# Kernel optimization log

Hardware: AMD Instinct MI355X
Metric: run time of the kernel (lower is better)

## Reference

```python
import jax, jax.numpy as jnp
import numpy as np

D_IN = 768
D_OUT = 768
N_HEADS = 12
HEAD_DIM = D_OUT // N_HEADS


def setup_inputs() -> dict:
    key = jax.random.key(0)
    ks = jax.random.split(key, 6)
    B, S = 2, 4096
    x = jax.random.normal(ks[0], (B, S, D_IN), dtype=jnp.float32)
    s = 0.02
    Wq = jax.random.normal(ks[1], (D_IN, D_OUT), dtype=jnp.float32) * s
    Wk = jax.random.normal(ks[2], (D_IN, D_OUT), dtype=jnp.float32) * s
    Wv = jax.random.normal(ks[3], (D_IN, D_OUT), dtype=jnp.float32) * s
    Wo = jax.random.normal(ks[4], (D_OUT, D_OUT), dtype=jnp.float32) * s
    bo = jnp.zeros((D_OUT,), dtype=jnp.float32)
    return {"x": x, "Wq": Wq, "Wk": Wk, "Wv": Wv, "Wo": Wo, "bo": bo}


def reference(x, Wq, Wk, Wv, Wo, bo):
    B, S, _ = x.shape
    # QKV projections (no bias), reshape to [B, H, S, Dh]
    q = (x @ Wq).reshape(B, S, N_HEADS, HEAD_DIM).transpose(0, 2, 1, 3)
    k = (x @ Wk).reshape(B, S, N_HEADS, HEAD_DIM).transpose(0, 2, 1, 3)
    v = (x @ Wv).reshape(B, S, N_HEADS, HEAD_DIM).transpose(0, 2, 1, 3)
    # scores: [B, H, S, S], causal mask, scaled softmax
    scores = jnp.einsum('bhqd,bhkd->bhqk', q, k)
    causal = jnp.triu(jnp.ones((S, S), dtype=bool), k=1)
    scores = jnp.where(causal, -jnp.inf, scores)
    attn = jax.nn.softmax(scores / np.sqrt(HEAD_DIM).astype(np.float32), axis=-1)
    # dropout p=0.0 -> identity
    ctx = jnp.einsum('bhqk,bhkd->bqhd', attn, v).reshape(B, S, D_OUT)
    return ctx @ Wo + bo
```

## Files before the change

### kernel.cpp

```cpp
#include <hip/hip_runtime.h>

#define S 4096
#define BATCH 2
#define D 768
#define NH 12
#define DH 64
#define NROWS (BATCH * S)
#define N_ITEMS (32 * NH * BATCH)
#define CTR_OFF 67633152

typedef __attribute__((ext_vector_type(8))) short bf16x8;
typedef __attribute__((ext_vector_type(4))) float f32x4;
typedef __attribute__((ext_vector_type(2))) unsigned uint32x2;

__device__ __forceinline__ unsigned short f2bf(float f) {
    unsigned u = __builtin_bit_cast(unsigned, f);
    u += 0x7fff + ((u >> 16) & 1);
    return (unsigned short)(u >> 16);
}

__device__ __forceinline__ float fexp2(float x) {
#if __has_builtin(__builtin_amdgcn_exp2f)
    return __builtin_amdgcn_exp2f(x);
#else
    return exp2f(x);
#endif
}

#define GLDS16(g, l)                                                   \
    __builtin_amdgcn_global_load_lds(                                  \
        (const __attribute__((address_space(1))) void*)(g),            \
        (__attribute__((address_space(3))) void*)(l), 16, 0, 0)

__global__ __launch_bounds__(256) void cvt_x(const float* __restrict__ x,
                                             unsigned short* __restrict__ xb)
{
    int i = (blockIdx.x * 256 + threadIdx.x) * 4;
    float4 v = *(const float4*)(x + i);
    ushort4 o = make_ushort4(f2bf(v.x), f2bf(v.y), f2bf(v.z), f2bf(v.w));
    *(ushort4*)(xb + i) = o;
}

__global__ __launch_bounds__(256) void cvt_w(
    const float* __restrict__ Wq, const float* __restrict__ Wk,
    const float* __restrict__ Wv, const float* __restrict__ Wo,
    unsigned short* __restrict__ wt)
{
    __shared__ float tile[32][33];
    const int z = blockIdx.z;
    const float* W = (z == 0) ? Wq : (z == 1) ? Wk : (z == 2) ? Wv : Wo;
    const int k0 = blockIdx.x * 32, n0 = blockIdx.y * 32;
    const int t = threadIdx.x;
    const int r = t >> 3, c4 = (t & 7) * 4;

    float4 v = *(const float4*)(W + (size_t)(k0 + r) * D + n0 + c4);
    tile[r][c4 + 0] = v.x; tile[r][c4 + 1] = v.y;
    tile[r][c4 + 2] = v.z; tile[r][c4 + 3] = v.w;
    __syncthreads();
    ushort4 o = make_ushort4(f2bf(tile[c4 + 0][r]), f2bf(tile[c4 + 1][r]),
                             f2bf(tile[c4 + 2][r]), f2bf(tile[c4 + 3][r]));
    *(ushort4*)(wt + ((size_t)z * D + n0 + r) * D + k0 + c4) = o;
}

__global__ __launch_bounds__(256) void gemm_qkv(
    const unsigned short* __restrict__ xb,
    const unsigned short* __restrict__ wt,
    unsigned short* __restrict__ qb, unsigned short* __restrict__ kb,
    unsigned short* __restrict__ vtb)
{
    __shared__ unsigned short As[128 * 64];
    __shared__ unsigned short Bs[128 * 64];

    const int t = threadIdx.x;
    const int lane = t & 63, w = t >> 6;
    const int l16 = lane & 15, quad = lane >> 4;
    const int wm = w & 1, wn = w >> 1;
    const int m0 = blockIdx.x * 128;
    const int n0g = blockIdx.y * 128;
    const int z = n0g / 768;
    const int c0 = n0g - z * 768;
    const unsigned short* Wz = wt + (size_t)z * D * D;

    f32x4 acc[4][4] = {};

    for (int k0 = 0; k0 < D; k0 += 64) {
#pragma unroll
        for (int i = 0; i < 4; ++i) {
            int g = i * 256 + w * 64 + lane;
            int row = g >> 3, cl = g & 7, cg = cl ^ (row & 7);
            GLDS16(xb + (size_t)(m0 + row) * D + k0 + cg * 8,
                   As + (size_t)(i * 256 + w * 64) * 8);
            GLDS16(Wz + (size_t)(c0 + row) * D + k0 + cg * 8,
                   Bs + (size_t)(i * 256 + w * 64) * 8);
        }
        __syncthreads();
#pragma unroll
        for (int kk = 0; kk < 2; ++kk) {
            bf16x8 af[4], bf_[4];
#pragma unroll
            for (int mt = 0; mt < 4; ++mt) {
                int r = wm * 64 + mt * 16 + l16;
                int c = kk * 4 + quad;
                af[mt] = *(const bf16x8*)&As[(r * 8 + (c ^ (r & 7))) * 8];
            }
#pragma unroll
            for (int nt = 0; nt < 4; ++nt) {
                int r = wn * 64 + nt * 16 + l16;
                int c = kk * 4 + quad;
                bf_[nt] = *(const bf16x8*)&Bs[(r * 8 + (c ^ (r & 7))) * 8];
            }
#pragma unroll
            for (int mt = 0; mt < 4; ++mt)
#pragma unroll
                for (int nt = 0; nt < 4; ++nt)
                    acc[mt][nt] = __builtin_amdgcn_mfma_f32_16x16x32_bf16(
                        af[mt], bf_[nt], acc[mt][nt], 0, 0, 0);
        }
        __syncthreads();
    }

    if (z < 2) {
        unsigned short* outp = (z == 0) ? qb : kb;
        const float scale = (z == 0) ? 0.18033688011112042f : 1.0f;
#pragma unroll
        for (int mt = 0; mt < 4; ++mt) {
#pragma unroll
            for (int reg = 0; reg < 4; ++reg) {
                int m = wm * 64 + mt * 16 + quad * 4 + reg;
                int ng = m0 + m;
                int b = ng >> 12, s = ng & 4095;
#pragma unroll
                for (int nt = 0; nt < 4; ++nt) {
                    int n = c0 + wn * 64 + nt * 16 + l16;
                    int h = n >> 6, dh = n & 63;
                    outp[(((size_t)b * NH + h) * S + s) * DH + dh] =
                        f2bf(acc[mt][nt][reg] * scale);
                }
            }
        }
    } else {
#pragma unroll
        for (int mt = 0; mt < 4; ++mt) {
#pragma unroll
            for (int nt = 0; nt < 4; ++nt) {
                int m = wm * 64 + mt * 16 + quad * 4;
                int ng = m0 + m;
                int b = ng >> 12, s = ng & 4095;
                int n = c0 + wn * 64 + nt * 16 + l16;
                int h = n >> 6, dh = n & 63;
                ushort4 p = make_ushort4(
                    f2bf(acc[mt][nt][0]), f2bf(acc[mt][nt][1]),
                    f2bf(acc[mt][nt][2]), f2bf(acc[mt][nt][3]));
                *(ushort4*)(vtb + (((size_t)b * NH + h) * DH + dh) * S + s) = p;
            }
        }
    }
}

__global__ __launch_bounds__(512, 4) void attn_mfma(
    const unsigned short* __restrict__ qg,
    const unsigned short* __restrict__ kg,
    const unsigned short* __restrict__ vtg,
    unsigned short* __restrict__ ctxb,
    int* __restrict__ work_ctr)
{
    __shared__ unsigned short Ks[2][64 * 64];
    __shared__ unsigned short Vs[2][64 * 64];
    __shared__ int s_item;

    const float INF = __builtin_inff();
    const int t = threadIdx.x;
    const int w = t >> 6, lane = t & 63;
    const int l16 = lane & 15, quad = lane >> 4;
    const int a7 = l16 & 7;
    const int srow = t >> 3;
    const int scg = (t & 7) ^ (srow & 7);

    bf16x8 vone;
#pragma unroll
    for (int i = 0; i < 8; ++i) vone[i] = (short)0x3F80;

    for (;;) {
        if (t == 0) s_item = atomicAdd(work_ctr, 1);
        __syncthreads();
        const int p = s_item;
        if (p >= N_ITEMS) return;

        const int qt = 31 - (p / (NH * BATCH));
        const int hb = p % (NH * BATCH);
        const int h = hb % NH, b = hb / NH;
        const size_t hbase = ((size_t)b * NH + h) * (size_t)S * DH;
        const unsigned short* kp = kg + hbase;
        const unsigned short* vp = vtg + hbase;

        const int qrow = qt * 128 + w * 16 + l16;
        bf16x8 bq[2];
#pragma unroll
        for (int kk = 0; kk < 2; ++kk)
            bq[kk] = *(const bf16x8*)(qg + hbase + (size_t)qrow * DH +
                                      kk * 32 + quad * 8);

        f32x4 acc_o[4] = {};
        f32x4 acc_sum = {};

        const int jmax = 2 * qt + 1, jd = 2 * qt;

        GLDS16(kp + (size_t)srow * DH + scg * 8, &Ks[0][(size_t)w * 64 * 8]);
        GLDS16(vp + (size_t)srow * S + scg * 8, &Vs[0][(size_t)w * 64 * 8]);

        for (int j = 0; j <= jmax; ++j) {
            const int cur = j & 1;
            __syncthreads();
            if (j < jmax) {
                GLDS16(kp + (size_t)((j + 1) * 64 + srow) * DH + scg * 8,
                       &Ks[cur ^ 1][(size_t)w * 64 * 8]);
                GLDS16(vp + (size_t)srow * S + (j + 1) * 64 + scg * 8,
                       &Vs[cur ^ 1][(size_t)w * 64 * 8]);
            }

            const unsigned short* Kc = Ks[cur];
            const unsigned short* Vc = Vs[cur];

            f32x4 acc_s[4] = {};
            __builtin_amdgcn_s_setprio(1);
#pragma unroll
            for (int kk = 0; kk < 2; ++kk)
#pragma unroll
                for (int ms = 0; ms < 4; ++ms) {
                    int r = ms * 16 + l16, c = kk * 4 + quad;
                    bf16x8 ak = *(const bf16x8*)&Kc[(r * 8 + (c ^ a7)) * 8];
                    acc_s[ms] = __builtin_amdgcn_mfma_f32_16x16x32_bf16(
                        ak, bq[kk], acc_s[ms], 0, 0, 0);
                }
            __builtin_amdgcn_s_setprio(0);

            if (j >= jd) {
#pragma unroll
                for (int ms = 0; ms < 4; ++ms)
#pragma unroll
                    for (int reg = 0; reg < 4; ++reg)
                        if ((j * 64 + ms * 16 + quad * 4 + reg) > qrow)
                            acc_s[ms][reg] = -INF;
            }

            bf16x8 bp[2];
            {
                unsigned ulo[4], uhi[4];
#pragma unroll
                for (int ms = 0; ms < 4; ++ms) {
                    float e0 = fexp2(acc_s[ms][0]);
                    float e1 = fexp2(acc_s[ms][1]);
                    float e2 = fexp2(acc_s[ms][2]);
                    float e3 = fexp2(acc_s[ms][3]);
                    asm("v_cvt_pk_bf16_f32 %0, %1, %2"
                        : "=v"(ulo[ms]) : "v"(e0), "v"(e1));
                    asm("v_cvt_pk_bf16_f32 %0, %1, %2"
                        : "=v"(uhi[ms]) : "v"(e2), "v"(e3));
                }
#pragma unroll
                for (int kp2 = 0; kp2 < 2; ++kp2) {
                    uint32x2 lo = __builtin_amdgcn_permlane32_swap(
                        ulo[2 * kp2], ulo[2 * kp2 + 1], false, false);
                    uint32x2 s02 = __builtin_amdgcn_permlane16_swap(
                        lo[0], lo[1], false, false);
                    uint32x2 hi = __builtin_amdgcn_permlane32_swap(
                        uhi[2 * kp2], uhi[2 * kp2 + 1], false, false);
                    uint32x2 s13 = __builtin_amdgcn_permlane16_swap(
                        hi[0], hi[1], false, false);
                    union { unsigned u[4]; bf16x8 v; } pb;
                    pb.u[0] = s02[0]; pb.u[1] = s13[0];
                    pb.u[2] = s02[1]; pb.u[3] = s13[1];
                    bp[kp2] = pb.v;
                }
            }

            __builtin_amdgcn_s_setprio(1);
#pragma unroll
            for (int kk = 0; kk < 2; ++kk) {
#pragma unroll
                for (int d = 0; d < 4; ++d) {
                    int r = d * 16 + l16, c = kk * 4 + quad;
                    bf16x8 av = *(const bf16x8*)&Vc[(r * 8 + (c ^ a7)) * 8];
                    acc_o[d] = __builtin_amdgcn_mfma_f32_16x16x32_bf16(
                        av, bp[kk], acc_o[d], 0, 0, 0);
                }
                acc_sum = __builtin_amdgcn_mfma_f32_16x16x32_bf16(
                    vone, bp[kk], acc_sum, 0, 0, 0);
            }
            __builtin_amdgcn_s_setprio(0);
        }

        {
            float inv = 1.f / acc_sum[0];
            size_t base = ((size_t)(b * S + qrow)) * D + h * 64;
#pragma unroll
            for (int d = 0; d < 4; ++d) {
                ushort4 o;
                o.x = f2bf(acc_o[d][0] * inv);
                o.y = f2bf(acc_o[d][1] * inv);
                o.z = f2bf(acc_o[d][2] * inv);
                o.w = f2bf(acc_o[d][3] * inv);
                *(ushort4*)(ctxb + base + d * 16 + quad * 4) = o;
            }
        }
    }
}

__global__ __launch_bounds__(256) void gemm_out(
    const unsigned short* __restrict__ ctxb,
    const unsigned short* __restrict__ wt,
    const float* __restrict__ bo,
    float* __restrict__ out)
{
    __shared__ unsigned short As[128 * 64];
    __shared__ unsigned short Bs[128 * 64];

    const int t = threadIdx.x;
    const int lane = t & 63, w = t >> 6;
    const int l16 = lane & 15, quad = lane >> 4;
    const int wm = w & 1, wn = w >> 1;
    const int m0 = blockIdx.x * 128;
    const int n0 = blockIdx.y * 128;
    const unsigned short* Wz = wt + (size_t)3 * D * D;

    f32x4 acc[4][4] = {};

    for (int k0 = 0; k0 < D; k0 += 64) {
#pragma unroll
        for (int i = 0; i < 4; ++i) {
            int g = i * 256 + w * 64 + lane;
            int row = g >> 3, cl = g & 7, cg = cl ^ (row & 7);
            GLDS16(ctxb + (size_t)(m0 + row) * D + k0 + cg * 8,
                   As + (size_t)(i * 256 + w * 64) * 8);
            GLDS16(Wz + (size_t)(n0 + row) * D + k0 + cg * 8,
                   Bs + (size_t)(i * 256 + w * 64) * 8);
        }
        __syncthreads();
#pragma unroll
        for (int kk = 0; kk < 2; ++kk) {
            bf16x8 af[4], bf_[4];
#pragma unroll
            for (int mt = 0; mt < 4; ++mt) {
                int r = wm * 64 + mt * 16 + l16;
                int c = kk * 4 + quad;
                af[mt] = *(const bf16x8*)&As[(r * 8 + (c ^ (r & 7))) * 8];
            }
#pragma unroll
            for (int nt = 0; nt < 4; ++nt) {
                int r = wn * 64 + nt * 16 + l16;
                int c = kk * 4 + quad;
                bf_[nt] = *(const bf16x8*)&Bs[(r * 8 + (c ^ (r & 7))) * 8];
            }
#pragma unroll
            for (int mt = 0; mt < 4; ++mt)
#pragma unroll
                for (int nt = 0; nt < 4; ++nt)
                    acc[mt][nt] = __builtin_amdgcn_mfma_f32_16x16x32_bf16(
                        af[mt], bf_[nt], acc[mt][nt], 0, 0, 0);
        }
        __syncthreads();
    }

    float bv[4];
#pragma unroll
    for (int nt = 0; nt < 4; ++nt)
        bv[nt] = bo[n0 + wn * 64 + nt * 16 + l16];
#pragma unroll
    for (int mt = 0; mt < 4; ++mt)
#pragma unroll
        for (int reg = 0; reg < 4; ++reg) {
            int m = m0 + wm * 64 + mt * 16 + quad * 4 + reg;
#pragma unroll
            for (int nt = 0; nt < 4; ++nt)
                out[(size_t)m * D + n0 + wn * 64 + nt * 16 + l16] =
                    acc[mt][nt][reg] + bv[nt];
        }
}

extern "C" void kernel_launch(void* const* d_in, const int* in_sizes, int n_in,
                              void* d_out, int out_size, void* d_ws, size_t ws_size,
                              hipStream_t stream)
{
    const float* x  = (const float*)d_in[0];
    const float* Wq = (const float*)d_in[1];
    const float* Wk = (const float*)d_in[2];
    const float* Wv = (const float*)d_in[3];
    const float* Wo = (const float*)d_in[4];
    const float* bo = (const float*)d_in[5];
    float* out = (float*)d_out;

    const size_t elems = (size_t)NROWS * D;
    unsigned short* xb   = (unsigned short*)d_ws;
    unsigned short* wt   = xb + elems;
    unsigned short* q    = wt + (size_t)4 * D * D;
    unsigned short* k    = q + elems;
    unsigned short* vt   = k + elems;
    unsigned short* ctxb = vt + elems;
    int* work_ctr = (int*)((char*)d_ws + CTR_OFF);

    hipMemsetAsync(work_ctr, 0, sizeof(int), stream);

    cvt_x<<<NROWS * D / 1024, 256, 0, stream>>>(x, xb);
    dim3 gw(D / 32, D / 32, 4);
    cvt_w<<<gw, 256, 0, stream>>>(Wq, Wk, Wv, Wo, wt);

    dim3 g1(NROWS / 128, (3 * D) / 128);
    gemm_qkv<<<g1, 256, 0, stream>>>(xb, wt, q, k, vt);

    attn_mfma<<<512, 512, 0, stream>>>(q, k, vt, ctxb, work_ctr);

    dim3 g3(NROWS / 128, D / 128);
    gemm_out<<<g3, 256, 0, stream>>>(ctxb, wt, bo, out);
}
```

Measured before the change: 234.1 us.

## Shrink attention work items to 64-row query tiles with 256-thread blocks

Each attention work item now covers 64 query rows with 4 waves instead of 128 rows with 8 waves, doubling the number of dynamically scheduled items. The grid grows to 1280 blocks of 256 threads, and the shared-memory work-index slot is folded into the K buffer with extra barriers. Finer causal tiles cut wasted masked work on the diagonal and give more even load balancing. The cost is that each K/V tile is loaded to shared memory once per 64 query rows rather than per 128, so global and LDS traffic per query rises, and each item pays more barriers.

```diff
diff --git a/kernel.cpp b/kernel.cpp
--- a/kernel.cpp
+++ b/kernel.cpp
@@ -6,7 +6,7 @@
 #define NH 12
 #define DH 64
 #define NROWS (BATCH * S)
-#define N_ITEMS (32 * NH * BATCH)
+#define N_ITEMS (64 * NH * BATCH)
 #define CTR_OFF 67633152
 
 typedef __attribute__((ext_vector_type(8))) short bf16x8;
@@ -157,7 +157,7 @@
     }
 }
 
-__global__ __launch_bounds__(512, 4) void attn_mfma(
+__global__ __launch_bounds__(256, 5) void attn_mfma(
     const unsigned short* __restrict__ qg,
     const unsigned short* __restrict__ kg,
     const unsigned short* __restrict__ vtg,
@@ -166,34 +166,35 @@
 {
     __shared__ unsigned short Ks[2][64 * 64];
     __shared__ unsigned short Vs[2][64 * 64];
-    __shared__ int s_item;
 
     const float INF = __builtin_inff();
     const int t = threadIdx.x;
     const int w = t >> 6, lane = t & 63;
     const int l16 = lane & 15, quad = lane >> 4;
     const int a7 = l16 & 7;
-    const int srow = t >> 3;
-    const int scg = (t & 7) ^ (srow & 7);
+    const int sg = t;
 
     bf16x8 vone;
 #pragma unroll
     for (int i = 0; i < 8; ++i) vone[i] = (short)0x3F80;
 
     for (;;) {
-        if (t == 0) s_item = atomicAdd(work_ctr, 1);
-        __syncthreads();
-        const int p = s_item;
+        __syncthreads();
+        if (t == 0)
+            *(volatile int*)&Ks[0][0] = atomicAdd(work_ctr, 1);
+        __syncthreads();
+        const int p = *(volatile int*)&Ks[0][0];
+        __syncthreads();
         if (p >= N_ITEMS) return;
 
-        const int qt = 31 - (p / (NH * BATCH));
+        const int qb = 63 - (p / (NH * BATCH));
         const int hb = p % (NH * BATCH);
         const int h = hb % NH, b = hb / NH;
         const size_t hbase = ((size_t)b * NH + h) * (size_t)S * DH;
         const unsigned short* kp = kg + hbase;
         const unsigned short* vp = vtg + hbase;
 
-        const int qrow = qt * 128 + w * 16 + l16;
+        const int qrow = qb * 64 + w * 16 + l16;
         bf16x8 bq[2];
 #pragma unroll
         for (int kk = 0; kk < 2; ++kk)
@@ -203,19 +204,31 @@
         f32x4 acc_o[4] = {};
         f32x4 acc_sum = {};
 
-        const int jmax = 2 * qt + 1, jd = 2 * qt;
-
-        GLDS16(kp + (size_t)srow * DH + scg * 8, &Ks[0][(size_t)w * 64 * 8]);
-        GLDS16(vp + (size_t)srow * S + scg * 8, &Vs[0][(size_t)w * 64 * 8]);
+        const int jmax = qb;
+
+#pragma unroll
+        for (int i = 0; i < 2; ++i) {
+            int g = i * 256 + sg;
+            int row = g >> 3, cg = (g & 7) ^ (row & 7);
+            GLDS16(kp + (size_t)row * DH + cg * 8,
+                   &Ks[0][(size_t)(i * 256 + w * 64) * 8]);
+            GLDS16(vp + (size_t)row * S + cg * 8,
+                   &Vs[0][(size_t)(i * 256 + w * 64) * 8]);
+        }
 
         for (int j = 0; j <= jmax; ++j) {
             const int cur = j & 1;
             __syncthreads();
             if (j < jmax) {
-                GLDS16(kp + (size_t)((j + 1) * 64 + srow) * DH + scg * 8,
-                       &Ks[cur ^ 1][(size_t)w * 64 * 8]);
-                GLDS16(vp + (size_t)srow * S + (j + 1) * 64 + scg * 8,
-                       &Vs[cur ^ 1][(size_t)w * 64 * 8]);
+#pragma unroll
+                for (int i = 0; i < 2; ++i) {
+                    int g = i * 256 + sg;
+                    int row = g >> 3, cg = (g & 7) ^ (row & 7);
+                    GLDS16(kp + (size_t)((j + 1) * 64 + row) * DH + cg * 8,
+                           &Ks[cur ^ 1][(size_t)(i * 256 + w * 64) * 8]);
+                    GLDS16(vp + (size_t)row * S + (j + 1) * 64 + cg * 8,
+                           &Vs[cur ^ 1][(size_t)(i * 256 + w * 64) * 8]);
+                }
             }
 
             const unsigned short* Kc = Ks[cur];
@@ -234,7 +247,7 @@
                 }
             __builtin_amdgcn_s_setprio(0);
 
-            if (j >= jd) {
+            if (j == jmax) {
 #pragma unroll
                 for (int ms = 0; ms < 4; ++ms)
 #pragma unroll
@@ -407,7 +420,7 @@
     dim3 g1(NROWS / 128, (3 * D) / 128);
     gemm_qkv<<<g1, 256, 0, stream>>>(xb, wt, q, k, vt);
 
-    attn_mfma<<<512, 512, 0, stream>>>(q, k, vt, ctxb, work_ctr);
+    attn_mfma<<<1280, 256, 0, stream>>>(q, k, vt, ctxb, work_ctr);
 
     dim3 g3(NROWS / 128, D / 128);
     gemm_out<<<g3, 256, 0, stream>>>(ctxb, wt, bo, out);
```

Result: slower. 259.8 us (+11.0%).
